# Kernel tuning notes

Hardware: AMD Instinct MI355X
Metric: run time of the kernel (lower is better)

## Reference

```python
import jax, jax.numpy as jnp
import numpy as np

EPS = 1e-6
K_MEM, C_MEM = 512, 2048
SEQ, BATCH = 256, 16
NUM_LAYERS, NUM_HEADS, HEAD_DIM = 12, 12, 64
KV_DIM = NUM_LAYERS * NUM_HEADS * HEAD_DIM * 2  # 18432
NOISE_STD = 0.01
PINV_STEPS = 3
BEN_COHEN_INIT = -5.0


def approx_pinv(A, steps=PINV_STEPS):
    # Ben-Cohen iterative pseudoinverse. A: (B, M, N) -> (B, N, M)
    alpha = jnp.minimum(jnp.exp(jnp.float32(BEN_COHEN_INIT)), jnp.float32(5e-4))  # clamp(max=5e-4)
    P = alpha * jnp.swapaxes(A, -2, -1)
    for _ in range(steps):
        P = 2.0 * P - (P @ A) @ P  # matches bmm(bmm(P, A), P)
    return P


def setup_inputs() -> dict:
    key = jax.random.key(0)
    ks = jax.random.split(key, 6)
    lim = np.sqrt(6.0 / (C_MEM + KV_DIM))  # xavier_uniform
    return {
        "z_sequence": jax.random.normal(ks[0], (SEQ, BATCH, C_MEM), jnp.float32),
        "z_query": jax.random.normal(ks[1], (BATCH, C_MEM), jnp.float32),
        "noise": jax.random.normal(ks[2], (SEQ, BATCH, C_MEM), jnp.float32),
        "memory_mean": jax.random.normal(ks[3], (K_MEM, C_MEM), jnp.float32) * 0.02,
        "memory_logvar": jnp.zeros((K_MEM,), jnp.float32),
        "w_logvar": jnp.zeros((1,), jnp.float32),
        "W_M_weight": jax.random.uniform(ks[4], (KV_DIM, C_MEM), jnp.float32, -lim, lim),
    }


def reference(z_sequence, z_query, noise, memory_mean, memory_logvar, w_logvar, W_M_weight):
    B = z_query.shape[0]
    # ---- write ----
    prior_var = jnp.exp(memory_logvar) + EPS                     # (K,)
    prior_mean_b = jnp.broadcast_to(memory_mean, (B, K_MEM, C_MEM))
    z_noise = z_sequence + noise * NOISE_STD                     # (S, B, C)
    z_t = jnp.swapaxes(z_noise, 0, 1)                            # (B, S, C)
    M_pinv = approx_pinv(prior_mean_b)                           # (B, C, K)
    w = z_t @ M_pinv                                             # (B, S, K)
    w_pinv = approx_pinv(w)                                      # (B, K, S)
    new_memory_mean = w_pinv @ z_t                               # (B, K, C)
    # KL divergence (post_var == prior_var here)
    t1 = C_MEM * jnp.sum(prior_var / prior_var)
    t2 = jnp.sum((new_memory_mean - prior_mean_b) ** 2 / prior_var[None, :, None], axis=(-2, -1))
    t3 = -jnp.float32(C_MEM * K_MEM)
    t4 = C_MEM * jnp.sum(jnp.log(prior_var) - jnp.log(prior_var))
    dkl_M = jnp.mean(t1 + t2 + t3 + t4)
    # ---- read (deterministic addressing) ----
    M_pinv2 = approx_pinv(new_memory_mean)                       # (B, C, K)
    w_mean = jnp.einsum('bc,bck->bk', z_query, M_pinv2)          # (B, K)
    z_retrieved = jnp.einsum('bk,bkc->bc', w_mean, new_memory_mean)  # (B, C)
    Z_r_kv = z_retrieved @ W_M_weight.T                          # (B, kv_dim)
    wl = jnp.broadcast_to(w_logvar, w_mean.shape)
    dkl_w = 0.5 * jnp.sum(jnp.exp(wl) + w_mean ** 2 - 1.0 - wl)
    return z_retrieved, Z_r_kv, dkl_M, dkl_w
```

## Files before the change

### kernel.cpp

```cpp
#include <hip/hip_runtime.h>

#define ALPHA 5.0e-4f

typedef short s16x8 __attribute__((ext_vector_type(8)));
typedef unsigned short u16x8 __attribute__((ext_vector_type(8)));
typedef float f32x4 __attribute__((ext_vector_type(4)));

__device__ __forceinline__ unsigned short f2bf(float f) {
    unsigned int u = __builtin_bit_cast(unsigned int, f);
    u += 0x7fffu + ((u >> 16) & 1u);
    return (unsigned short)(u >> 16);
}
__device__ __forceinline__ float bf2f(unsigned short h) {
    return __builtin_bit_cast(float, (unsigned int)h << 16);
}
__device__ __forceinline__ f32x4 mfma16(s16x8 a, s16x8 b, f32x4 c) {
    return __builtin_amdgcn_mfma_f32_16x16x32_bf16(a, b, c, 0, 0, 0);
}

template<int ROWS>
__device__ __forceinline__ void stage_kcontig(const float* __restrict__ src, int ld,
                                              unsigned short* __restrict__ lds, int tid)
{
#pragma unroll
    for (int it = 0; it < ROWS * 8 / 256; ++it) {
        const int g = tid + it * 256;
        const int row = g >> 3, s = g & 7;
        const float* p = src + (long long)row * ld + s * 8;
        const float4 x0 = *(const float4*)p;
        const float4 x1 = *(const float4*)(p + 4);
        u16x8 h;
        h[0] = f2bf(x0.x); h[1] = f2bf(x0.y); h[2] = f2bf(x0.z); h[3] = f2bf(x0.w);
        h[4] = f2bf(x1.x); h[5] = f2bf(x1.y); h[6] = f2bf(x1.z); h[7] = f2bf(x1.w);
        *(u16x8*)(lds + row * 64 + ((s ^ (row & 7)) << 3)) = h;
    }
}

template<int ROWS>
__device__ __forceinline__ void stage_kstrided(const float* __restrict__ src, int ld,
                                               unsigned short* __restrict__ lds, int tid)
{
    constexpr int KPT = ROWS * 64 / 256;
    const int m = tid % ROWS, kb = (tid / ROWS) * KPT;
#pragma unroll
    for (int j8 = 0; j8 < KPT / 8; ++j8) {
        u16x8 h;
#pragma unroll
        for (int j = 0; j < 8; ++j)
            h[j] = f2bf(src[(long long)(kb + j8 * 8 + j) * ld + m]);
        const int s = (kb >> 3) + j8;
        *(u16x8*)(lds + m * 64 + ((s ^ (m & 7)) << 3)) = h;
    }
}

template<int ROWS>
__device__ __forceinline__ void stage_kcontig_b(const unsigned short* __restrict__ src, int ld,
                                                unsigned short* __restrict__ lds, int tid)
{
#pragma unroll
    for (int it = 0; it < ROWS * 8 / 256; ++it) {
        const int g = tid + it * 256;
        const int row = g >> 3, s = g & 7;
        const u16x8 h = *(const u16x8*)(src + (long long)row * ld + s * 8);
        *(u16x8*)(lds + row * 64 + ((s ^ (row & 7)) << 3)) = h;
    }
}

template<int ROWS>
__device__ __forceinline__ void stage_kstrided_b(const unsigned short* __restrict__ src, int ld,
                                                 unsigned short* __restrict__ lds, int tid)
{
    constexpr int KPT = ROWS * 64 / 256;
    const int m = tid % ROWS, kb = (tid / ROWS) * KPT;
#pragma unroll
    for (int j8 = 0; j8 < KPT / 8; ++j8) {
        u16x8 h;
#pragma unroll
        for (int j = 0; j < 8; ++j)
            h[j] = src[(long long)(kb + j8 * 8 + j) * ld + m];
        const int s = (kb >> 3) + j8;
        *(u16x8*)(lds + m * 64 + ((s ^ (m & 7)) << 3)) = h;
    }
}

template<int BM, int BN, bool TA, bool TB, bool ABF, bool BBF, bool OBF,
         bool OT, bool CINT, bool ATOM = false>
__device__ __forceinline__
void gemm_dev(int bx, int by, int bz,
              const void* __restrict__ Av, int lda, long long sA,
              const void* __restrict__ Bv, int ldb, long long sB,
              void* __restrict__ Dv, int ldd, long long sD,
              const float* __restrict__ Cin, long long sC,
              float alpha, float beta, int Kd)
{
    constexpr int TWM = BM / 2, TWN = BN / 2;
    constexpr int FM = TWM / 16, FN = TWN / 16;
    __shared__ unsigned short As[BM * 64];
    __shared__ unsigned short Bs[BN * 64];

    const int tid = threadIdx.x;
    const int lane = tid & 63, w = tid >> 6;
    const int wm = w >> 1, wn = w & 1;
    const int lrow = lane & 15, lk = lane >> 4;
    const int m0 = by * BM, n0 = bx * BN;

    f32x4 acc[FM][FN];
#pragma unroll
    for (int i = 0; i < FM; ++i)
#pragma unroll
        for (int j = 0; j < FN; ++j) acc[i][j] = (f32x4){0.f, 0.f, 0.f, 0.f};

    for (int k0 = 0; k0 < Kd; k0 += 64) {
        if (ABF) {
            const unsigned short* Ab = (const unsigned short*)Av + (long long)bz * sA;
            if (!TA) stage_kcontig_b<BM>(Ab + (long long)m0 * lda + k0, lda, As, tid);
            else     stage_kstrided_b<BM>(Ab + (long long)k0 * lda + m0, lda, As, tid);
        } else {
            const float* Ab = (const float*)Av + (long long)bz * sA;
            if (!TA) stage_kcontig<BM>(Ab + (long long)m0 * lda + k0, lda, As, tid);
            else     stage_kstrided<BM>(Ab + (long long)k0 * lda + m0, lda, As, tid);
        }
        if (BBF) {
            const unsigned short* Bb = (const unsigned short*)Bv + (long long)bz * sB;
            if (TB)  stage_kcontig_b<BN>(Bb + (long long)n0 * ldb + k0, ldb, Bs, tid);
            else     stage_kstrided_b<BN>(Bb + (long long)k0 * ldb + n0, ldb, Bs, tid);
        } else {
            const float* Bb = (const float*)Bv + (long long)bz * sB;
            if (TB)  stage_kcontig<BN>(Bb + (long long)n0 * ldb + k0, ldb, Bs, tid);
            else     stage_kstrided<BN>(Bb + (long long)k0 * ldb + n0, ldb, Bs, tid);
        }
        __syncthreads();
#pragma unroll
        for (int kk = 0; kk < 2; ++kk) {
            s16x8 ah[FM], bh[FN];
#pragma unroll
            for (int i = 0; i < FM; ++i) {
                const int row = wm * TWM + i * 16 + lrow;
                const int s = kk * 4 + lk;
                ah[i] = *(const s16x8*)(As + row * 64 + ((s ^ (row & 7)) << 3));
            }
#pragma unroll
            for (int j = 0; j < FN; ++j) {
                const int col = wn * TWN + j * 16 + lrow;
                const int s = kk * 4 + lk;
                bh[j] = *(const s16x8*)(Bs + col * 64 + ((s ^ (col & 7)) << 3));
            }
#pragma unroll
            for (int i = 0; i < FM; ++i)
#pragma unroll
                for (int j = 0; j < FN; ++j)
                    acc[i][j] = mfma16(ah[i], bh[j], acc[i][j]);
        }
        __syncthreads();
    }

#pragma unroll
    for (int i = 0; i < FM; ++i)
#pragma unroll
        for (int j = 0; j < FN; ++j) {
            const int col = n0 + wn * TWN + j * 16 + lrow;
#pragma unroll
            for (int r = 0; r < 4; ++r) {
                const int row = m0 + wm * TWM + i * 16 + lk * 4 + r;
                float v = alpha * acc[i][j][r];
                if (Cin) {
                    const float cv = CINT ? Cin[(long long)col * sC + row]
                                          : Cin[(long long)row * ldd + col];
                    v = fmaf(beta, cv, v);
                }
                if (ATOM) {
                    atomicAdd((float*)Dv + (long long)row * ldd + col, v);
                } else if (OT) {
                    ((unsigned short*)Dv)[(long long)(row >> 8) * sD +
                                          (long long)col * ldd + (row & 255)] = f2bf(v);
                } else if (OBF) {
                    ((unsigned short*)Dv + (long long)bz * sD)[(long long)row * ldd + col] = f2bf(v);
                } else {
                    ((float*)Dv + (long long)bz * sD)[(long long)row * ldd + col] = v;
                }
            }
        }
}

template<int BM, int BN, bool TA, bool TB, bool ABF, bool BBF, bool OBF,
         bool OT = false, bool CINT = false>
__global__ __launch_bounds__(256)
void gemm_mfma(const void* __restrict__ Av, int lda, long long sA,
               const void* __restrict__ Bv, int ldb, long long sB,
               void* __restrict__ Dv, int ldd, long long sD,
               const float* __restrict__ Cin, long long sC,
               float alpha, float beta, int Kd)
{
    gemm_dev<BM, BN, TA, TB, ABF, BBF, OBF, OT, CINT>(
        blockIdx.x, blockIdx.y, blockIdx.z,
        Av, lda, sA, Bv, ldb, sB, Dv, ldd, sD, Cin, sC, alpha, beta, Kd);
}

__global__ __launch_bounds__(256)
void fused_prep_kernel(const float* __restrict__ zs, const float* __restrict__ no,
                       const float* __restrict__ zq, const float* __restrict__ mm,
                       unsigned short* __restrict__ ztb, float* __restrict__ q,
                       float* __restrict__ G1)
{
    const int blk = blockIdx.x, t = threadIdx.x;
    if (blk < 4096) {
        const int bs = blk;
        const int b = bs >> 8, sI = bs & 255;
        const long long in = ((long long)sI * 16 + b) * 2048 + t * 8;
        const f32x4 z0 = __builtin_nontemporal_load((const f32x4*)(zs + in));
        const f32x4 z1 = __builtin_nontemporal_load((const f32x4*)(zs + in + 4));
        const f32x4 n0 = __builtin_nontemporal_load((const f32x4*)(no + in));
        const f32x4 n1 = __builtin_nontemporal_load((const f32x4*)(no + in + 4));
        float zf[8];
#pragma unroll
        for (int j = 0; j < 4; ++j) {
            zf[j]     = fmaf(0.01f, n0[j], z0[j]);
            zf[j + 4] = fmaf(0.01f, n1[j], z1[j]);
        }
        u16x8 o;
#pragma unroll
        for (int j = 0; j < 8; ++j) o[j] = f2bf(zf[j]);
        *(u16x8*)(ztb + ((long long)bs * 2048 + t * 8)) = o;
        const float4 q0 = *(const float4*)(zq + b * 2048 + t * 8);
        const float4 q1 = *(const float4*)(zq + b * 2048 + t * 8 + 4);
        float qa = zf[0] * q0.x + zf[1] * q0.y + zf[2] * q0.z + zf[3] * q0.w
                 + zf[4] * q1.x + zf[5] * q1.y + zf[6] * q1.z + zf[7] * q1.w;
        __shared__ float red[256];
        red[t] = qa; __syncthreads();
        for (int st = 128; st > 0; st >>= 1) { if (t < st) red[t] += red[t + st]; __syncthreads(); }
        if (t == 0) q[bs] = red[0];
    } else {
        const int g = blk - 4096;
        const int ky = g & 7;
        const int tile = g >> 3;
        gemm_dev<64, 64, false, true, false, false, false, false, false, true>(
            tile & 7, tile >> 3, 0,
            mm + ky * 256, 2048, 0, mm + ky * 256, 2048, 0,
            G1, 512, 0, nullptr, 0, 1.f, 0.f, 256);
    }
}

__global__ __launch_bounds__(256)
void wT_u_kernel(const unsigned short* __restrict__ ztb,
                 const unsigned short* __restrict__ P1b,
                 unsigned short* __restrict__ wTb,
                 const float* __restrict__ q, float* __restrict__ wmean)
{
    constexpr int BM = 128, BN = 64, TWM = 64, TWN = 32, FM = 4, FN = 2;
    __shared__ unsigned short As[BM * 64];
    __shared__ unsigned short Bs[BN * 64];
    const int lin = blockIdx.x;
    const int r = lin & 7, tt = lin >> 3;
    const int by = r + 8 * (tt & 3), bx = tt >> 2;
    const int tid = threadIdx.x;
    const int lane = tid & 63, w = tid >> 6;
    const int wm = w >> 1, wn = w & 1;
    const int lrow = lane & 15, lk = lane >> 4;
    const int m0 = by * BM, n0 = bx * BN;

    f32x4 acc[FM][FN];
#pragma unroll
    for (int i = 0; i < FM; ++i)
#pragma unroll
        for (int j = 0; j < FN; ++j) acc[i][j] = (f32x4){0.f, 0.f, 0.f, 0.f};

    for (int k0 = 0; k0 < 2048; k0 += 64) {
        stage_kcontig_b<BM>(ztb + (long long)m0 * 2048 + k0, 2048, As, tid);
        stage_kstrided_b<BN>(P1b + (long long)k0 * 512 + n0, 512, Bs, tid);
        __syncthreads();
#pragma unroll
        for (int kk = 0; kk < 2; ++kk) {
            s16x8 ah[FM], bh[FN];
#pragma unroll
            for (int i = 0; i < FM; ++i) {
                const int row = wm * TWM + i * 16 + lrow;
                const int s = kk * 4 + lk;
                ah[i] = *(const s16x8*)(As + row * 64 + ((s ^ (row & 7)) << 3));
            }
#pragma unroll
            for (int j = 0; j < FN; ++j) {
                const int col = wn * TWN + j * 16 + lrow;
                const int s = kk * 4 + lk;
                bh[j] = *(const s16x8*)(Bs + col * 64 + ((s ^ (col & 7)) << 3));
            }
#pragma unroll
            for (int i = 0; i < FM; ++i)
#pragma unroll
                for (int j = 0; j < FN; ++j)
                    acc[i][j] = mfma16(ah[i], bh[j], acc[i][j]);
        }
        __syncthreads();
    }

    float up[FN] = {0.f, 0.f};
#pragma unroll
    for (int i = 0; i < FM; ++i)
#pragma unroll
        for (int rr = 0; rr < 4; ++rr) {
            const int row = m0 + wm * TWM + i * 16 + lk * 4 + rr;
            const float qv = q[row];
#pragma unroll
            for (int j = 0; j < FN; ++j) {
                const int col = n0 + wn * TWN + j * 16 + lrow;
                const float v = acc[i][j][rr];
                wTb[(long long)(row >> 8) * 131072 + (long long)col * 256 + (row & 255)] = f2bf(v);
                up[j] = fmaf(v, qv, up[j]);
            }
        }
    const int b = m0 >> 8;
#pragma unroll
    for (int j = 0; j < FN; ++j) {
        float v = up[j];
        v += __shfl_xor(v, 16);
        v += __shfl_xor(v, 32);
        if (lk == 0) {
            const int col = n0 + wn * TWN + j * 16 + lrow;
            atomicAdd(&wmean[b * 512 + col], (64.0f * ALPHA * ALPHA) * v);
        }
    }
}

__global__ __launch_bounds__(256)
void tail_kernel(const unsigned short* __restrict__ wTb,
                 const unsigned short* __restrict__ ztb,
                 const float* __restrict__ mm, const float* __restrict__ mlv,
                 const float* __restrict__ wmean, const float* __restrict__ wlv,
                 float* __restrict__ out)
{
    __shared__ __align__(16) unsigned char smem[34304];
    const int blk = blockIdx.x, tid = threadIdx.x;
    if (blk < 1024) {
        constexpr int BM = 128, BN = 128, TWM = 64, TWN = 64, FM = 4, FN = 4;
        unsigned short* As = (unsigned short*)smem;
        unsigned short* Bs = As + BM * 64;
        float* ivars = (float*)(smem + 32768);
        float* red = (float*)(smem + 33280);
        const int r8 = blk & 7, t8 = blk >> 3;
        const int bz = r8 + 8 * (t8 & 1);
        const int rest = t8 >> 1;
        const int by = rest & 3, bx = rest >> 2;
        const int lane = tid & 63, w = tid >> 6;
        const int wm = w >> 1, wn = w & 1;
        const int lrow = lane & 15, lk = lane >> 4;
        const int m0 = by * BM, n0 = bx * BN;

        if (tid < 128) ivars[tid] = 1.0f / (expf(mlv[m0 + tid]) + 1e-6f);

        f32x4 acc[FM][FN];
#pragma unroll
        for (int i = 0; i < FM; ++i)
#pragma unroll
            for (int j = 0; j < FN; ++j) acc[i][j] = (f32x4){0.f, 0.f, 0.f, 0.f};

        for (int k0 = 0; k0 < 256; k0 += 64) {
            stage_kcontig_b<BM>(wTb + (long long)bz * 131072 + (long long)m0 * 256 + k0, 256, As, tid);
            stage_kstrided_b<BN>(ztb + (long long)bz * 524288 + (long long)k0 * 2048 + n0, 2048, Bs, tid);
            __syncthreads();
#pragma unroll
            for (int kk = 0; kk < 2; ++kk) {
                s16x8 ah[FM], bh[FN];
#pragma unroll
                for (int i = 0; i < FM; ++i) {
                    const int row = wm * TWM + i * 16 + lrow;
                    const int s = kk * 4 + lk;
                    ah[i] = *(const s16x8*)(As + row * 64 + ((s ^ (row & 7)) << 3));
                }
#pragma unroll
                for (int j = 0; j < FN; ++j) {
                    const int col = wn * TWN + j * 16 + lrow;
                    const int s = kk * 4 + lk;
                    bh[j] = *(const s16x8*)(Bs + col * 64 + ((s ^ (col & 7)) << 3));
                }
#pragma unroll
                for (int i = 0; i < FM; ++i)
#pragma unroll
                    for (int j = 0; j < FN; ++j)
                        acc[i][j] = mfma16(ah[i], bh[j], acc[i][j]);
            }
            __syncthreads();
        }

        const float A8 = 8.0f * ALPHA;
        float da = 0.f;
#pragma unroll
        for (int i = 0; i < FM; ++i)
#pragma unroll
            for (int j = 0; j < FN; ++j) {
                const int cl = wn * TWN + j * 16 + lrow;
#pragma unroll
                for (int rr = 0; rr < 4; ++rr) {
                    const int rl = wm * TWM + i * 16 + lk * 4 + rr;
                    const float v = A8 * acc[i][j][rr];
                    const float d = v - mm[(long long)(m0 + rl) * 2048 + (n0 + cl)];
                    da = fmaf(d * d, ivars[rl], da);
                }
            }
        red[tid] = da; __syncthreads();
        for (int st = 128; st > 0; st >>= 1) { if (tid < st) red[tid] += red[tid + st]; __syncthreads(); }
        if (tid == 0) atomicAdd(&out[327680], red[0] * (1.0f / 16.0f));
    } else if (blk < 1280) {
        float* wms = (float*)smem;
        float* ys  = (float*)(smem + 2048);
        float* red2 = (float*)(smem + 3072);
        const int idx = blk - 1024;
        const int r8 = idx & 7, t8 = idx >> 3;
        const int b = r8 + 8 * (t8 & 1), ct = t8 >> 1;
        wms[tid] = wmean[b * 512 + tid];
        wms[tid + 256] = wmean[b * 512 + 256 + tid];
        __syncthreads();
        {
            const unsigned short* wp = wTb + (long long)b * 131072 + tid;
            float yv = 0.f;
#pragma unroll 8
            for (int k = 0; k < 512; ++k)
                yv = fmaf(wms[k], bf2f(wp[(long long)k * 256]), yv);
            ys[tid] = yv;
        }
        __syncthreads();
        const int c = ct * 128 + (tid & 127), sh = tid >> 7;
        const unsigned short* zp = ztb + (long long)b * 524288 + c;
        float acc2 = 0.f;
        const int sbase = sh * 128;
#pragma unroll 8
        for (int s = 0; s < 128; ++s)
            acc2 = fmaf(ys[sbase + s], bf2f(zp[(long long)(sbase + s) * 2048]), acc2);
        red2[tid] = acc2; __syncthreads();
        if (sh == 0)
            out[(long long)b * 2048 + c] = (8.0f * ALPHA) * (red2[tid] + red2[tid + 128]);
    } else {
        float* red = (float*)smem;
        float s = 0.f;
        for (int i = tid; i < 16 * 512; i += 256) { const float v = wmean[i]; s += v * v; }
        red[tid] = s; __syncthreads();
        for (int st = 128; st > 0; st >>= 1) { if (tid < st) red[tid] += red[tid + st]; __syncthreads(); }
        if (tid == 0) {
            const float l = wlv[0];
            out[327681] = 0.5f * (red[0] + 8192.0f * (expf(l) - 1.0f - l));
        }
    }
}

__global__ __launch_bounds__(256)
void zrkv_mfma_kernel(const float* __restrict__ W, const float* __restrict__ zr,
                      float* __restrict__ part)
{
    const int tid = threadIdx.x, lane = tid & 63, w = tid >> 6;
    const int bx = blockIdx.x, ky = blockIdx.y;
    const int d0 = bx * 64 + w * 16;
    const int kc0 = ky * 256;
    const int rr = lane & 15, kq = lane >> 4;
    s16x8 areg[8];
    const float* zb = zr + rr * 2048 + kc0 + kq * 8;
#pragma unroll
    for (int s = 0; s < 8; ++s) {
        const f32x4 a0 = *(const f32x4*)(zb + s * 32);
        const f32x4 a1 = *(const f32x4*)(zb + s * 32 + 4);
        u16x8 h;
#pragma unroll
        for (int j = 0; j < 4; ++j) { h[j] = f2bf(a0[j]); h[j + 4] = f2bf(a1[j]); }
        areg[s] = __builtin_bit_cast(s16x8, h);
    }
    f32x4 acc = {0.f, 0.f, 0.f, 0.f};
    const float* wb = W + (long long)(d0 + rr) * 2048 + kc0 + kq * 8;
#pragma unroll
    for (int s = 0; s < 8; ++s) {
        const f32x4 b0 = __builtin_nontemporal_load((const f32x4*)(wb + s * 32));
        const f32x4 b1 = __builtin_nontemporal_load((const f32x4*)(wb + s * 32 + 4));
        u16x8 h;
#pragma unroll
        for (int j = 0; j < 4; ++j) { h[j] = f2bf(b0[j]); h[j + 4] = f2bf(b1[j]); }
        acc = mfma16(areg[s], __builtin_bit_cast(s16x8, h), acc);
    }
    float* pb = part + (((long long)ky * 288 + bx) * 4 + w) * 256 + kq * 64 + rr;
#pragma unroll
    for (int r = 0; r < 4; ++r) pb[r * 16] = acc[r];
}

__global__ __launch_bounds__(256)
void zrkv_combine_kernel(const float* __restrict__ part, float* __restrict__ out)
{
    const int b = blockIdx.y;
    const int d = blockIdx.x * 256 + threadIdx.x;
    const int base = ((d >> 6) * 4 + ((d >> 4) & 3)) * 256 + b * 16 + (d & 15);
    float s = 0.f;
#pragma unroll
    for (int ky = 0; ky < 8; ++ky)
        s += part[(long long)ky * 294912 + base];
    out[(long long)b * 18432 + d] = s;
}

extern "C" void kernel_launch(void* const* d_in, const int* in_sizes, int n_in,
                              void* d_out, int out_size, void* d_ws, size_t ws_size,
                              hipStream_t stream)
{
    (void)in_sizes; (void)n_in; (void)out_size; (void)ws_size;
    const float* z_seq   = (const float*)d_in[0];
    const float* z_query = (const float*)d_in[1];
    const float* noise   = (const float*)d_in[2];
    const float* mm      = (const float*)d_in[3];
    const float* mlv     = (const float*)d_in[4];
    const float* wlv     = (const float*)d_in[5];
    const float* WM      = (const float*)d_in[6];
    float* out = (float*)d_out;

    char* wsb = (char*)d_ws;
    unsigned short* ztb  = (unsigned short*)(wsb);
    unsigned short* wTb  = (unsigned short*)(wsb + (16LL << 20));
    float*          G1   = (float*)(wsb + (24LL << 20));
    unsigned short* P1b  = (unsigned short*)(wsb + (26LL << 20));
    float*          pZ   = (float*)(wsb + (40LL << 20));
    float*          vec  = (float*)(wsb + (52LL << 20));
    float* qvec     = vec;
    float* wmean    = vec + 4096;

    hipMemsetAsync(G1, 0, 512 * 512 * sizeof(float), stream);
    hipMemsetAsync(wmean, 0, 8192 * sizeof(float), stream);
    hipMemsetAsync(out + 327680, 0, sizeof(float), stream);
    fused_prep_kernel<<<4608, 256, 0, stream>>>(z_seq, noise, z_query, mm,
                                                ztb, qvec, G1);
    gemm_mfma<64,64,true,false,false,false,true,false,true><<<dim3(8,32,1),256,0,stream>>>(
        mm,2048,0, G1,512,0, P1b,512,0, mm,2048,
        -28.0f*ALPHA*ALPHA, 8.0f*ALPHA, 512);
    wT_u_kernel<<<256,256,0,stream>>>(ztb, P1b, wTb, qvec, wmean);
    tail_kernel<<<1281,256,0,stream>>>(wTb, ztb, mm, mlv, wmean, wlv, out);
    zrkv_mfma_kernel<<<dim3(288,8),256,0,stream>>>(WM, out, pZ);
    zrkv_combine_kernel<<<dim3(72,16),256,0,stream>>>(pZ, out + 32768);
}
```

Baseline: 181.4 us.

## Split tail kernel and co-schedule KL GEMM with Z_r_kv projection using atomics

The tail is split in two kernels. One computes z_retrieved and dkl_w. The second interleaves the KL-divergence GEMM blocks with the Z_r_kv MFMA blocks in one grid, so the compute-bound GEMM overlaps the memory-bound W_M stream. The separate partial-sum buffer and combine kernel are replaced by float atomicAdd into a pre-zeroed output region, and the memsets are merged into fewer calls. This removes one launch and a partials round trip. In exchange it adds atomic traffic, and the summation order of Z_r_kv becomes nondeterministic.

```diff
diff --git a/kernel.cpp b/kernel.cpp
--- a/kernel.cpp
+++ b/kernel.cpp
@@ -321,89 +321,18 @@
 }
 
 __global__ __launch_bounds__(256)
-void tail_kernel(const unsigned short* __restrict__ wTb,
-                 const unsigned short* __restrict__ ztb,
-                 const float* __restrict__ mm, const float* __restrict__ mlv,
-                 const float* __restrict__ wmean, const float* __restrict__ wlv,
-                 float* __restrict__ out)
-{
-    __shared__ __align__(16) unsigned char smem[34304];
+void tail1_kernel(const unsigned short* __restrict__ wTb,
+                  const unsigned short* __restrict__ ztb,
+                  const float* __restrict__ wmean, const float* __restrict__ wlv,
+                  float* __restrict__ out)
+{
+    __shared__ __align__(16) float smemf[1024];
     const int blk = blockIdx.x, tid = threadIdx.x;
-    if (blk < 1024) {
-        constexpr int BM = 128, BN = 128, TWM = 64, TWN = 64, FM = 4, FN = 4;
-        unsigned short* As = (unsigned short*)smem;
-        unsigned short* Bs = As + BM * 64;
-        float* ivars = (float*)(smem + 32768);
-        float* red = (float*)(smem + 33280);
+    if (blk < 256) {
+        float* wms = smemf;
+        float* ys  = smemf + 512;
+        float* red2 = smemf + 768;
         const int r8 = blk & 7, t8 = blk >> 3;
-        const int bz = r8 + 8 * (t8 & 1);
-        const int rest = t8 >> 1;
-        const int by = rest & 3, bx = rest >> 2;
-        const int lane = tid & 63, w = tid >> 6;
-        const int wm = w >> 1, wn = w & 1;
-        const int lrow = lane & 15, lk = lane >> 4;
-        const int m0 = by * BM, n0 = bx * BN;
-
-        if (tid < 128) ivars[tid] = 1.0f / (expf(mlv[m0 + tid]) + 1e-6f);
-
-        f32x4 acc[FM][FN];
-#pragma unroll
-        for (int i = 0; i < FM; ++i)
-#pragma unroll
-            for (int j = 0; j < FN; ++j) acc[i][j] = (f32x4){0.f, 0.f, 0.f, 0.f};
-
-        for (int k0 = 0; k0 < 256; k0 += 64) {
-            stage_kcontig_b<BM>(wTb + (long long)bz * 131072 + (long long)m0 * 256 + k0, 256, As, tid);
-            stage_kstrided_b<BN>(ztb + (long long)bz * 524288 + (long long)k0 * 2048 + n0, 2048, Bs, tid);
-            __syncthreads();
-#pragma unroll
-            for (int kk = 0; kk < 2; ++kk) {
-                s16x8 ah[FM], bh[FN];
-#pragma unroll
-                for (int i = 0; i < FM; ++i) {
-                    const int row = wm * TWM + i * 16 + lrow;
-                    const int s = kk * 4 + lk;
-                    ah[i] = *(const s16x8*)(As + row * 64 + ((s ^ (row & 7)) << 3));
-                }
-#pragma unroll
-                for (int j = 0; j < FN; ++j) {
-                    const int col = wn * TWN + j * 16 + lrow;
-                    const int s = kk * 4 + lk;
-                    bh[j] = *(const s16x8*)(Bs + col * 64 + ((s ^ (col & 7)) << 3));
-                }
-#pragma unroll
-                for (int i = 0; i < FM; ++i)
-#pragma unroll
-                    for (int j = 0; j < FN; ++j)
-                        acc[i][j] = mfma16(ah[i], bh[j], acc[i][j]);
-            }
-            __syncthreads();
-        }
-
-        const float A8 = 8.0f * ALPHA;
-        float da = 0.f;
-#pragma unroll
-        for (int i = 0; i < FM; ++i)
-#pragma unroll
-            for (int j = 0; j < FN; ++j) {
-                const int cl = wn * TWN + j * 16 + lrow;
-#pragma unroll
-                for (int rr = 0; rr < 4; ++rr) {
-                    const int rl = wm * TWM + i * 16 + lk * 4 + rr;
-                    const float v = A8 * acc[i][j][rr];
-                    const float d = v - mm[(long long)(m0 + rl) * 2048 + (n0 + cl)];
-                    da = fmaf(d * d, ivars[rl], da);
-                }
-            }
-        red[tid] = da; __syncthreads();
-        for (int st = 128; st > 0; st >>= 1) { if (tid < st) red[tid] += red[tid + st]; __syncthreads(); }
-        if (tid == 0) atomicAdd(&out[327680], red[0] * (1.0f / 16.0f));
-    } else if (blk < 1280) {
-        float* wms = (float*)smem;
-        float* ys  = (float*)(smem + 2048);
-        float* red2 = (float*)(smem + 3072);
-        const int idx = blk - 1024;
-        const int r8 = idx & 7, t8 = idx >> 3;
         const int b = r8 + 8 * (t8 & 1), ct = t8 >> 1;
         wms[tid] = wmean[b * 512 + tid];
         wms[tid + 256] = wmean[b * 512 + 256 + tid];
@@ -428,7 +357,7 @@
         if (sh == 0)
             out[(long long)b * 2048 + c] = (8.0f * ALPHA) * (red2[tid] + red2[tid + 128]);
     } else {
-        float* red = (float*)smem;
+        float* red = smemf;
         float s = 0.f;
         for (int i = tid; i < 16 * 512; i += 256) { const float v = wmean[i]; s += v * v; }
         red[tid] = s; __syncthreads();
@@ -441,52 +370,117 @@
 }
 
 __global__ __launch_bounds__(256)
-void zrkv_mfma_kernel(const float* __restrict__ W, const float* __restrict__ zr,
-                      float* __restrict__ part)
-{
-    const int tid = threadIdx.x, lane = tid & 63, w = tid >> 6;
-    const int bx = blockIdx.x, ky = blockIdx.y;
-    const int d0 = bx * 64 + w * 16;
-    const int kc0 = ky * 256;
-    const int rr = lane & 15, kq = lane >> 4;
-    s16x8 areg[8];
-    const float* zb = zr + rr * 2048 + kc0 + kq * 8;
-#pragma unroll
-    for (int s = 0; s < 8; ++s) {
-        const f32x4 a0 = *(const f32x4*)(zb + s * 32);
-        const f32x4 a1 = *(const f32x4*)(zb + s * 32 + 4);
-        u16x8 h;
-#pragma unroll
-        for (int j = 0; j < 4; ++j) { h[j] = f2bf(a0[j]); h[j + 4] = f2bf(a1[j]); }
-        areg[s] = __builtin_bit_cast(s16x8, h);
-    }
-    f32x4 acc = {0.f, 0.f, 0.f, 0.f};
-    const float* wb = W + (long long)(d0 + rr) * 2048 + kc0 + kq * 8;
-#pragma unroll
-    for (int s = 0; s < 8; ++s) {
-        const f32x4 b0 = __builtin_nontemporal_load((const f32x4*)(wb + s * 32));
-        const f32x4 b1 = __builtin_nontemporal_load((const f32x4*)(wb + s * 32 + 4));
-        u16x8 h;
-#pragma unroll
-        for (int j = 0; j < 4; ++j) { h[j] = f2bf(b0[j]); h[j + 4] = f2bf(b1[j]); }
-        acc = mfma16(areg[s], __builtin_bit_cast(s16x8, h), acc);
-    }
-    float* pb = part + (((long long)ky * 288 + bx) * 4 + w) * 256 + kq * 64 + rr;
-#pragma unroll
-    for (int r = 0; r < 4; ++r) pb[r * 16] = acc[r];
-}
-
-__global__ __launch_bounds__(256)
-void zrkv_combine_kernel(const float* __restrict__ part, float* __restrict__ out)
-{
-    const int b = blockIdx.y;
-    const int d = blockIdx.x * 256 + threadIdx.x;
-    const int base = ((d >> 6) * 4 + ((d >> 4) & 3)) * 256 + b * 16 + (d & 15);
-    float s = 0.f;
-#pragma unroll
-    for (int ky = 0; ky < 8; ++ky)
-        s += part[(long long)ky * 294912 + base];
-    out[(long long)b * 18432 + d] = s;
+void tail2_kernel(const unsigned short* __restrict__ wTb,
+                  const unsigned short* __restrict__ ztb,
+                  const float* __restrict__ mm, const float* __restrict__ mlv,
+                  const float* __restrict__ WM, float* __restrict__ out)
+{
+    __shared__ __align__(16) unsigned char smem[34304];
+    const int g = blockIdx.x, tid = threadIdx.x;
+    const int grp = g / 26, p = g % 26;
+    if (p < 8) {
+        constexpr int BM = 128, BN = 128, TWM = 64, TWN = 64, FM = 4, FN = 4;
+        unsigned short* As = (unsigned short*)smem;
+        unsigned short* Bs = As + BM * 64;
+        float* ivars = (float*)(smem + 32768);
+        float* red = (float*)(smem + 33280);
+        const int bz = ((2 * grp + p) & 7) + 8 * (grp & 1);
+        const int rest = grp >> 1;
+        const int by = rest & 3, bx = rest >> 2;
+        const int lane = tid & 63, w = tid >> 6;
+        const int wm = w >> 1, wn = w & 1;
+        const int lrow = lane & 15, lk = lane >> 4;
+        const int m0 = by * BM, n0 = bx * BN;
+
+        if (tid < 128) ivars[tid] = 1.0f / (expf(mlv[m0 + tid]) + 1e-6f);
+
+        f32x4 acc[FM][FN];
+#pragma unroll
+        for (int i = 0; i < FM; ++i)
+#pragma unroll
+            for (int j = 0; j < FN; ++j) acc[i][j] = (f32x4){0.f, 0.f, 0.f, 0.f};
+
+        for (int k0 = 0; k0 < 256; k0 += 64) {
+            stage_kcontig_b<BM>(wTb + (long long)bz * 131072 + (long long)m0 * 256 + k0, 256, As, tid);
+            stage_kstrided_b<BN>(ztb + (long long)bz * 524288 + (long long)k0 * 2048 + n0, 2048, Bs, tid);
+            __syncthreads();
+#pragma unroll
+            for (int kk = 0; kk < 2; ++kk) {
+                s16x8 ah[FM], bh[FN];
+#pragma unroll
+                for (int i = 0; i < FM; ++i) {
+                    const int row = wm * TWM + i * 16 + lrow;
+                    const int s = kk * 4 + lk;
+                    ah[i] = *(const s16x8*)(As + row * 64 + ((s ^ (row & 7)) << 3));
+                }
+#pragma unroll
+                for (int j = 0; j < FN; ++j) {
+                    const int col = wn * TWN + j * 16 + lrow;
+                    const int s = kk * 4 + lk;
+                    bh[j] = *(const s16x8*)(Bs + col * 64 + ((s ^ (col & 7)) << 3));
+                }
+#pragma unroll
+                for (int i = 0; i < FM; ++i)
+#pragma unroll
+                    for (int j = 0; j < FN; ++j)
+                        acc[i][j] = mfma16(ah[i], bh[j], acc[i][j]);
+            }
+            __syncthreads();
+        }
+
+        const float A8 = 8.0f * ALPHA;
+        float da = 0.f;
+#pragma unroll
+        for (int i = 0; i < FM; ++i)
+#pragma unroll
+            for (int j = 0; j < FN; ++j) {
+                const int cl = wn * TWN + j * 16 + lrow;
+#pragma unroll
+                for (int rr = 0; rr < 4; ++rr) {
+                    const int rl = wm * TWM + i * 16 + lk * 4 + rr;
+                    const float v = A8 * acc[i][j][rr];
+                    const float d = v - mm[(long long)(m0 + rl) * 2048 + (n0 + cl)];
+                    da = fmaf(d * d, ivars[rl], da);
+                }
+            }
+        red[tid] = da; __syncthreads();
+        for (int st = 128; st > 0; st >>= 1) { if (tid < st) red[tid] += red[tid + st]; __syncthreads(); }
+        if (tid == 0) atomicAdd(&out[327680], red[0] * (1.0f / 16.0f));
+    } else {
+        const int z = grp * 18 + (p - 8);
+        const int bx = z % 288, ky = z / 288;
+        const int lane = tid & 63, w = tid >> 6;
+        const int d0 = bx * 64 + w * 16;
+        const int kc0 = ky * 256;
+        const int rr = lane & 15, kq = lane >> 4;
+        const float* zr = out;
+        s16x8 areg[8];
+        const float* zb = zr + rr * 2048 + kc0 + kq * 8;
+#pragma unroll
+        for (int s = 0; s < 8; ++s) {
+            const f32x4 a0 = *(const f32x4*)(zb + s * 32);
+            const f32x4 a1 = *(const f32x4*)(zb + s * 32 + 4);
+            u16x8 h;
+#pragma unroll
+            for (int j = 0; j < 4; ++j) { h[j] = f2bf(a0[j]); h[j + 4] = f2bf(a1[j]); }
+            areg[s] = __builtin_bit_cast(s16x8, h);
+        }
+        f32x4 acc = {0.f, 0.f, 0.f, 0.f};
+        const float* wb = WM + (long long)(d0 + rr) * 2048 + kc0 + kq * 8;
+#pragma unroll
+        for (int s = 0; s < 8; ++s) {
+            const f32x4 b0 = __builtin_nontemporal_load((const f32x4*)(wb + s * 32));
+            const f32x4 b1 = __builtin_nontemporal_load((const f32x4*)(wb + s * 32 + 4));
+            u16x8 h;
+#pragma unroll
+            for (int j = 0; j < 4; ++j) { h[j] = f2bf(b0[j]); h[j + 4] = f2bf(b1[j]); }
+            acc = mfma16(areg[s], __builtin_bit_cast(s16x8, h), acc);
+        }
+        float* oz = out + 32768;
+#pragma unroll
+        for (int r = 0; r < 4; ++r)
+            atomicAdd(&oz[(long long)(kq * 4 + r) * 18432 + d0 + rr], acc[r]);
+    }
 }
 
 extern "C" void kernel_launch(void* const* d_in, const int* in_sizes, int n_in,
@@ -507,22 +501,18 @@
     unsigned short* ztb  = (unsigned short*)(wsb);
     unsigned short* wTb  = (unsigned short*)(wsb + (16LL << 20));
     float*          G1   = (float*)(wsb + (24LL << 20));
+    float*          wmean = (float*)(wsb + (25LL << 20));
     unsigned short* P1b  = (unsigned short*)(wsb + (26LL << 20));
-    float*          pZ   = (float*)(wsb + (40LL << 20));
-    float*          vec  = (float*)(wsb + (52LL << 20));
-    float* qvec     = vec;
-    float* wmean    = vec + 4096;
-
-    hipMemsetAsync(G1, 0, 512 * 512 * sizeof(float), stream);
-    hipMemsetAsync(wmean, 0, 8192 * sizeof(float), stream);
-    hipMemsetAsync(out + 327680, 0, sizeof(float), stream);
+    float*          qvec = (float*)(wsb + (30LL << 20));
+
+    hipMemsetAsync(G1, 0, (1u << 20) + 32768, stream);
+    hipMemsetAsync(out + 32768, 0, (294912 + 1) * sizeof(float), stream);
     fused_prep_kernel<<<4608, 256, 0, stream>>>(z_seq, noise, z_query, mm,
                                                 ztb, qvec, G1);
     gemm_mfma<64,64,true,false,false,false,true,false,true><<<dim3(8,32,1),256,0,stream>>>(
         mm,2048,0, G1,512,0, P1b,512,0, mm,2048,
         -28.0f*ALPHA*ALPHA, 8.0f*ALPHA, 512);
     wT_u_kernel<<<256,256,0,stream>>>(ztb, P1b, wTb, qvec, wmean);
-    tail_kernel<<<1281,256,0,stream>>>(wTb, ztb, mm, mlv, wmean, wlv, out);
-    zrkv_mfma_kernel<<<dim3(288,8),256,0,stream>>>(WM, out, pZ);
-    zrkv_combine_kernel<<<dim3(72,16),256,0,stream>>>(pZ, out + 32768);
-}
+    tail1_kernel<<<257,256,0,stream>>>(wTb, ztb, wmean, wlv, out);
+    tail2_kernel<<<3328,256,0,stream>>>(wTb, ztb, mm, mlv, WM, out);
+}
```

Result: faster. 177.6 us (-2.1%).
